# Optimization experiments

Hardware: AMD Instinct MI355X
Metric: run time of the kernel (lower is better)

## Reference

```python
import jax, jax.numpy as jnp
import numpy as np

NV = 100000   # vehicle nodes
NE = 100000   # 'edge' nodes (dst type)
E = 250000    # graph edges (connects relation)
VDIM = 16
EDIM = 16
HID = 128
HEADS = 4
DH = 128      # out_feats per head (GATv2Conv(hid, hid))
EPS = 1e-5
NEG_SLOPE = 0.2


def _layernorm(x, g, b):
    mu = x.mean(-1, keepdims=True)
    var = ((x - mu) ** 2).mean(-1, keepdims=True)
    return (x - mu) * jax.lax.rsqrt(var + EPS) * g + b


def setup_inputs() -> dict:
    key = jax.random.key(0)
    ks = jax.random.split(key, 20)
    s = 0.05
    return {
        "v_feat": jax.random.normal(ks[0], (NV, VDIM), jnp.float32),
        "e_feat": jax.random.normal(ks[1], (NE, EDIM), jnp.float32),
        "Wv": jax.random.normal(ks[2], (VDIM, HID), jnp.float32) * s,
        "bv": jnp.zeros((HID,), jnp.float32),
        "gv": jnp.ones((HID,), jnp.float32),
        "betav": jnp.zeros((HID,), jnp.float32),
        "We": jax.random.normal(ks[3], (EDIM, HID), jnp.float32) * s,
        "be": jnp.zeros((HID,), jnp.float32),
        "ge": jnp.ones((HID,), jnp.float32),
        "betae": jnp.zeros((HID,), jnp.float32),
        "Wsrc": jax.random.normal(ks[4], (HID, HEADS * DH), jnp.float32) * s,
        "bsrc": jnp.zeros((HEADS * DH,), jnp.float32),
        "Wdst": jax.random.normal(ks[5], (HID, HEADS * DH), jnp.float32) * s,
        "bdst": jnp.zeros((HEADS * DH,), jnp.float32),
        "attn": jax.random.normal(ks[6], (HEADS, DH), jnp.float32) * s,
        "Wp": jax.random.normal(ks[7], (HID, HID), jnp.float32) * s,
        "bp": jnp.zeros((HID,), jnp.float32),
        "src": jax.random.randint(ks[8], (E,), 0, NV, jnp.int32),
        "dst": jax.random.randint(ks[9], (E,), 0, NE, jnp.int32),
    }


def reference(v_feat, e_feat, Wv, bv, gv, betav, We, be, ge, betae,
              Wsrc, bsrc, Wdst, bdst, attn, Wp, bp, src, dst):
    # --- node-type encoders: Linear -> ReLU -> LayerNorm ---
    h_v = _layernorm(jax.nn.relu(v_feat @ Wv + bv), gv, betav)      # [NV, HID]
    h_e = _layernorm(jax.nn.relu(e_feat @ We + be), ge, betae)      # [NE, HID]

    # --- GATv2Conv (bipartite: vehicle -> edge), 4 heads ---
    fs = (h_v @ Wsrc + bsrc).reshape(NV, HEADS, DH)                 # src proj
    fd = (h_e @ Wdst + bdst).reshape(NE, HEADS, DH)                 # dst proj
    e = jax.nn.leaky_relu(fs[src] + fd[dst], NEG_SLOPE)             # [E, H, D]
    score = jnp.einsum("ehd,hd->eh", e, attn)                       # [E, H]
    # segment-wise (per-dst-node) softmax over incoming edges
    smax = jax.ops.segment_max(score, dst, num_segments=NE)         # [NE, H]
    ex = jnp.exp(score - smax[dst])
    denom = jax.ops.segment_sum(ex, dst, num_segments=NE)
    alpha = ex / denom[dst]                                         # [E, H]
    out = jax.ops.segment_sum(alpha[:, :, None] * fs[src], dst,
                              num_segments=NE)                      # [NE, H, D]

    # HeteroGraphConv mean-aggregate (single relation -> identity),
    # then mean over heads (edge_out.dim()==3 branch)
    edge_out = out.mean(axis=1)                                     # [NE, HID]

    # feature_proj: Linear -> ReLU -> Dropout(eval: identity)
    return jax.nn.relu(edge_out @ Wp + bp)
```

## Files before the change

kernel.cpp:

```cpp
#include <hip/hip_runtime.h>
#include <hip/hip_bf16.h>
#include <math.h>

#define NV 100000
#define NE_N 100000
#define NEDGE 250000
#define NPAD 100032
#define NEG 0.2f
#define LN_EPS 1e-5f

typedef __bf16 bf16_t;
typedef __bf16 bf16x8 __attribute__((ext_vector_type(8)));
typedef float f32x4 __attribute__((ext_vector_type(4)));
typedef float f32x2 __attribute__((ext_vector_type(2)));

__device__ inline unsigned short f2bfu(float f) {
    return __builtin_bit_cast(unsigned short, (__bf16)f);
}
__device__ inline float blo(unsigned w) { return __uint_as_float(w << 16); }
__device__ inline float bhi(unsigned w) { return __uint_as_float(w & 0xffff0000u); }
__device__ inline float lrelu(float x) { return x > 0.f ? x : NEG * x; }
__device__ inline unsigned pk2(float a, float b) {
    return (unsigned)f2bfu(a) | ((unsigned)f2bfu(b) << 16);
}

__device__ __forceinline__ void gload_lds16(const void* g, void* l) {
    __builtin_amdgcn_global_load_lds(
        (const __attribute__((address_space(1))) unsigned int*)g,
        (__attribute__((address_space(3))) unsigned int*)l,
        16, 0, 0);
}

__global__ __launch_bounds__(256) void prep_kernel(
    const float* __restrict__ Wsrc, const float* __restrict__ Wdst,
    const float* __restrict__ Wp, bf16_t* __restrict__ pS,
    bf16_t* __restrict__ pD, bf16_t* __restrict__ pP,
    int* __restrict__ deg)
{
    int t = blockIdx.x * 256 + threadIdx.x;
    if (t < 8192) {
        int ksq = t >> 9, col = t & 511;
#pragma unroll
        for (int j = 0; j < 8; ++j)
            pS[(size_t)t * 8 + j] = (bf16_t)Wsrc[(ksq * 8 + j) * 512 + col];
    } else if (t < 16384) {
        int g = t - 8192;
        int ksq = g >> 9, col = g & 511;
#pragma unroll
        for (int j = 0; j < 8; ++j)
            pD[(size_t)g * 8 + j] = (bf16_t)Wdst[(ksq * 8 + j) * 512 + col];
    } else if (t < 18432) {
        int g = t - 16384;
        int ksq = g >> 7, col = g & 127;
#pragma unroll
        for (int j = 0; j < 8; ++j)
            pP[(size_t)g * 8 + j] = (bf16_t)Wp[(ksq * 8 + j) * 128 + col];
    } else {
        int z = t - 18432;
        if (z < NE_N) deg[z] = 0;
    }
}

__global__ __launch_bounds__(256) void count_kernel(
    const int* __restrict__ dst, int* __restrict__ deg)
{
    int t = blockIdx.x * 256 + threadIdx.x;
    if (t < NEDGE) atomicAdd(&deg[dst[t]], 1);
}

__global__ __launch_bounds__(256) void scan1_kernel(
    const int* __restrict__ deg, int* __restrict__ offs, int* __restrict__ bsum)
{
    __shared__ int s[256];
    int i = blockIdx.x * 256 + threadIdx.x;
    int v = (i < NE_N) ? deg[i] : 0;
    s[threadIdx.x] = v;
    __syncthreads();
    for (int off = 1; off < 256; off <<= 1) {
        int t_ = (threadIdx.x >= off) ? s[threadIdx.x - off] : 0;
        __syncthreads();
        s[threadIdx.x] += t_;
        __syncthreads();
    }
    if (i < NE_N) offs[i] = s[threadIdx.x] - v;
    if (threadIdx.x == 255) bsum[blockIdx.x] = s[255];
}

__global__ __launch_bounds__(512) void scan2_kernel(int* __restrict__ bsum, int nb)
{
    __shared__ int s[512];
    int t = threadIdx.x;
    int v = (t < nb) ? bsum[t] : 0;
    s[t] = v;
    __syncthreads();
    for (int off = 1; off < 512; off <<= 1) {
        int t_ = (t >= off) ? s[t - off] : 0;
        __syncthreads();
        s[t] += t_;
        __syncthreads();
    }
    if (t < nb) bsum[t] = s[t] - v;
}

__global__ __launch_bounds__(256) void scan3_kernel(
    int* __restrict__ offs, const int* __restrict__ bsum,
    int* __restrict__ cursor, const int* __restrict__ deg,
    int2* __restrict__ od)
{
    int i = blockIdx.x * 256 + threadIdx.x;
    if (i < NE_N) {
        int o = offs[i] + bsum[blockIdx.x];
        offs[i] = o;
        cursor[i] = o;
        od[i] = make_int2(o, deg[i]);
    }
}

__global__ __launch_bounds__(256) void scatter_kernel(
    const int* __restrict__ dst, const int* __restrict__ src,
    int* __restrict__ cursor, int* __restrict__ srcs)
{
    int t = blockIdx.x * 256 + threadIdx.x;
    if (t < NEDGE) {
        int pos = atomicAdd(&cursor[dst[t]], 1);
        srcs[pos] = src[t];
    }
}

__global__ __launch_bounds__(256, 4) void enc_proj_kernel(
    const float* __restrict__ featV, const float* __restrict__ WencV,
    const float* __restrict__ bencV, const float* __restrict__ gV,
    const float* __restrict__ betaV, const bf16_t* __restrict__ ApackV,
    const float* __restrict__ bprojV, unsigned short* __restrict__ outV,
    const float* __restrict__ featE, const float* __restrict__ WencE,
    const float* __restrict__ bencE, const float* __restrict__ gE,
    const float* __restrict__ betaE, const bf16_t* __restrict__ ApackE,
    const float* __restrict__ bprojE, unsigned short* __restrict__ outE,
    int nblk1, int M)
{
    __shared__ unsigned short Hs[64 * 136];
    __shared__ __align__(16) unsigned short Abuf[2][8192];
    __shared__ __align__(16) float Bias[512];

    int b = blockIdx.x;
    bool isV = b < nblk1;
    const float* feat  = isV ? featV  : featE;
    const float* Wenc  = isV ? WencV  : WencE;
    const float* benc  = isV ? bencV  : bencE;
    const float* gln   = isV ? gV     : gE;
    const float* beta  = isV ? betaV  : betaE;
    const bf16_t* Apack = isV ? ApackV : ApackE;
    const float* bproj = isV ? bprojV : bprojE;
    unsigned short* out = isV ? outV : outE;
    int row0 = (isV ? b : b - nblk1) * 64;

    int t = threadIdx.x;
    int l = t & 63;
    int w = t >> 6;
    int rbase = __builtin_amdgcn_readfirstlane(w * 16);

    {
        int sr = row0 + rbase + (l >> 2);
        if (sr > M - 1) sr = M - 1;
        gload_lds16(feat + (size_t)sr * 16 + (l & 3) * 4, &Abuf[1][w * 512]);
    }

#pragma unroll
    for (int j = 0; j < 4; ++j) {
        int ksq = w * 4 + j;
        gload_lds16(Apack + ((size_t)(ksq * 512) + l) * 8, &Abuf[0][ksq * 512]);
    }
    if (t < 128)
        *(float4*)&Bias[t * 4] = *(const float4*)(bproj + t * 4);

    f32x2 wc2[16];
#pragma unroll
    for (int k = 0; k < 16; ++k) {
        float2 wv = *(const float2*)(Wenc + k * 128 + 2 * l);
        wc2[k][0] = wv.x;
        wc2[k][1] = wv.y;
    }
    float2 bv2 = *(const float2*)(benc + 2 * l);

    asm volatile("s_waitcnt vmcnt(0)" ::: "memory");

    const float* Fs = (const float*)&Abuf[1][0];
#pragma unroll
    for (int i = 0; i < 16; ++i) {
        const float* fr = Fs + (rbase + i) * 16;
        float4 f0 = *(const float4*)(fr);
        float4 f1 = *(const float4*)(fr + 4);
        float4 f2 = *(const float4*)(fr + 8);
        float4 f3 = *(const float4*)(fr + 12);
        f32x2 a = {bv2.x, bv2.y};
        a = __builtin_elementwise_fma((f32x2)f0.x, wc2[0],  a);
        a = __builtin_elementwise_fma((f32x2)f0.y, wc2[1],  a);
        a = __builtin_elementwise_fma((f32x2)f0.z, wc2[2],  a);
        a = __builtin_elementwise_fma((f32x2)f0.w, wc2[3],  a);
        a = __builtin_elementwise_fma((f32x2)f1.x, wc2[4],  a);
        a = __builtin_elementwise_fma((f32x2)f1.y, wc2[5],  a);
        a = __builtin_elementwise_fma((f32x2)f1.z, wc2[6],  a);
        a = __builtin_elementwise_fma((f32x2)f1.w, wc2[7],  a);
        a = __builtin_elementwise_fma((f32x2)f2.x, wc2[8],  a);
        a = __builtin_elementwise_fma((f32x2)f2.y, wc2[9],  a);
        a = __builtin_elementwise_fma((f32x2)f2.z, wc2[10], a);
        a = __builtin_elementwise_fma((f32x2)f2.w, wc2[11], a);
        a = __builtin_elementwise_fma((f32x2)f3.x, wc2[12], a);
        a = __builtin_elementwise_fma((f32x2)f3.y, wc2[13], a);
        a = __builtin_elementwise_fma((f32x2)f3.z, wc2[14], a);
        a = __builtin_elementwise_fma((f32x2)f3.w, wc2[15], a);
        float a0 = fmaxf(a[0], 0.f);
        float a1 = fmaxf(a[1], 0.f);
        *(unsigned*)&Hs[(rbase + i) * 136 + 2 * l] = pk2(a0, a1);
    }

    float s = 0.f, s2 = 0.f;
    {
        int rr = rbase + (l >> 2);
        int q = l & 3;
#pragma unroll
        for (int j = 0; j < 4; ++j) {
            uint4 v = *(const uint4*)&Hs[rr * 136 + q * 32 + j * 8];
            float x;
            x = blo(v.x); s += x; s2 = fmaf(x, x, s2);
            x = bhi(v.x); s += x; s2 = fmaf(x, x, s2);
            x = blo(v.y); s += x; s2 = fmaf(x, x, s2);
            x = bhi(v.y); s += x; s2 = fmaf(x, x, s2);
            x = blo(v.z); s += x; s2 = fmaf(x, x, s2);
            x = bhi(v.z); s += x; s2 = fmaf(x, x, s2);
            x = blo(v.w); s += x; s2 = fmaf(x, x, s2);
            x = bhi(v.w); s += x; s2 = fmaf(x, x, s2);
        }
    }
    s  += __shfl_xor(s, 1, 64);  s  += __shfl_xor(s, 2, 64);
    s2 += __shfl_xor(s2, 1, 64); s2 += __shfl_xor(s2, 2, 64);
    float mu  = s * (1.f / 128.f);
    float var = s2 * (1.f / 128.f) - mu * mu;
    float inv = rsqrtf(var + LN_EPS);

    int kq = l >> 4;
    int ln = l & 15;
    float mu_r  = __shfl(mu,  ln * 4, 64);
    float inv_r = __shfl(inv, ln * 4, 64);

    bf16x8 bfr[4];
#pragma unroll
    for (int ks = 0; ks < 4; ++ks) {
        int c0 = ks * 32 + kq * 8;
        uint4 v = *(const uint4*)&Hs[(rbase + ln) * 136 + c0];
        float4 g0 = *(const float4*)(gln + c0);
        float4 g1 = *(const float4*)(gln + c0 + 4);
        float4 b0 = *(const float4*)(beta + c0);
        float4 b1 = *(const float4*)(beta + c0 + 4);
        uint4 p;
        p.x = pk2(fmaf((blo(v.x) - mu_r) * inv_r, g0.x, b0.x),
                  fmaf((bhi(v.x) - mu_r) * inv_r, g0.y, b0.y));
        p.y = pk2(fmaf((blo(v.y) - mu_r) * inv_r, g0.z, b0.z),
                  fmaf((bhi(v.y) - mu_r) * inv_r, g0.w, b0.w));
        p.z = pk2(fmaf((blo(v.z) - mu_r) * inv_r, g1.x, b1.x),
                  fmaf((bhi(v.z) - mu_r) * inv_r, g1.y, b1.y));
        p.w = pk2(fmaf((blo(v.w) - mu_r) * inv_r, g1.z, b1.z),
                  fmaf((bhi(v.w) - mu_r) * inv_r, g1.w, b1.w));
        bfr[ks] = __builtin_bit_cast(bf16x8, p);
    }

    unsigned short* stag = Hs + rbase * 136;
    int node = row0 + rbase + ln;

#pragma unroll
    for (int p = 0; p < 8; ++p) {
        if (p == 0)
            asm volatile("s_waitcnt lgkmcnt(0)" ::: "memory");
        else
            asm volatile("s_waitcnt vmcnt(2)" ::: "memory");
        __builtin_amdgcn_s_barrier();

        if (p < 7) {
#pragma unroll
            for (int j = 0; j < 4; ++j) {
                int ksq = w * 4 + j;
                gload_lds16(Apack + ((size_t)(ksq * 512 + (p + 1) * 64) + l) * 8,
                            &Abuf[(p + 1) & 1][ksq * 512]);
            }
            __builtin_amdgcn_sched_barrier(0);
        }

        const unsigned short* Ac = Abuf[p & 1];
#pragma unroll
        for (int mt = 0; mt < 4; ++mt) {
            bf16x8 a[4];
#pragma unroll
            for (int ks = 0; ks < 4; ++ks)
                a[ks] = *(const bf16x8*)&Ac[((ks * 4 + kq) * 64 + mt * 16 + ln) * 8];

            f32x4 acc = {0.f, 0.f, 0.f, 0.f};
#pragma unroll
            for (int ks = 0; ks < 4; ++ks)
                acc = __builtin_amdgcn_mfma_f32_16x16x32_bf16(a[ks], bfr[ks], acc, 0, 0, 0);

            int colp = p * 64 + mt * 16 + kq * 4;
            float4 bb = *(const float4*)&Bias[colp];
            ushort4 o;
            o.x = f2bfu(acc[0] + bb.x);
            o.y = f2bfu(acc[1] + bb.y);
            o.z = f2bfu(acc[2] + bb.z);
            o.w = f2bfu(acc[3] + bb.w);
            *(ushort4*)&stag[ln * 136 + mt * 16 + kq * 4] = o;
        }
#pragma unroll
        for (int i = 0; i < 2; ++i) {
            uint4 v = *(const uint4*)&stag[ln * 136 + i * 32 + kq * 8];
            *(uint4*)(out + (size_t)node * 512 + p * 64 + i * 32 + kq * 8) = v;
        }
    }
}

__global__ __launch_bounds__(256) void final_gemm_kernel(
    const float* __restrict__ A, const unsigned short* __restrict__ Abf,
    const bf16_t* __restrict__ Ppack, const float* __restrict__ bp,
    float* __restrict__ C, int M)
{
    __shared__ unsigned short Hs[64 * 136];
    int t = threadIdx.x;
    int lane = t & 63;
    int w = t >> 6;
    int row0 = blockIdx.x * 64;

    if (Abf) {
#pragma unroll
        for (int i = 0; i < 4; ++i) {
            int idx = i * 256 + t;
            int r = idx >> 4;
            int c = (idx & 15) * 8;
            uint4 v = make_uint4(0, 0, 0, 0);
            if (row0 + r < M)
                v = *(const uint4*)(Abf + (size_t)(row0 + r) * 128 + c);
            *(uint4*)&Hs[r * 136 + c] = v;
        }
    } else {
#pragma unroll
        for (int i = 0; i < 8; ++i) {
            int f4 = i * 256 + t;
            int r = f4 >> 5;
            int c4 = (f4 & 31) * 4;
            float4 v = make_float4(0.f, 0.f, 0.f, 0.f);
            if (row0 + r < M)
                v = ((const float4*)(A + (size_t)(row0 + r) * 128))[f4 & 31];
            ushort4 o;
            o.x = f2bfu(v.x); o.y = f2bfu(v.y); o.z = f2bfu(v.z); o.w = f2bfu(v.w);
            *(ushort4*)&Hs[r * 136 + c4] = o;
        }
    }
    __syncthreads();

    int kq = lane >> 4;
    int ln = lane & 15;

    f32x4 acc[2][4];
#pragma unroll
    for (int mt = 0; mt < 2; ++mt)
#pragma unroll
        for (int nt = 0; nt < 4; ++nt) {
            f32x4 z = {0.f, 0.f, 0.f, 0.f};
            acc[mt][nt] = z;
        }

#pragma unroll
    for (int ks = 0; ks < 4; ++ks) {
        bf16x8 bfr[4];
#pragma unroll
        for (int nt = 0; nt < 4; ++nt) {
            const uint4* p = (const uint4*)&Hs[(nt * 16 + ln) * 136 + ks * 32 + kq * 8];
            bfr[nt] = __builtin_bit_cast(bf16x8, *p);
        }
        bf16x8 afr[2];
#pragma unroll
        for (int mt = 0; mt < 2; ++mt) {
            int colA = w * 32 + mt * 16 + ln;
            afr[mt] = *(const bf16x8*)(Ppack + ((size_t)(ks * 4 + kq) * 128 + colA) * 8);
        }
#pragma unroll
        for (int mt = 0; mt < 2; ++mt)
#pragma unroll
            for (int nt = 0; nt < 4; ++nt)
                acc[mt][nt] = __builtin_amdgcn_mfma_f32_16x16x32_bf16(
                    afr[mt], bfr[nt], acc[mt][nt], 0, 0, 0);
    }

#pragma unroll
    for (int mt = 0; mt < 2; ++mt) {
        int col = w * 32 + mt * 16 + kq * 4;
        float4 bb = *(const float4*)(bp + col);
#pragma unroll
        for (int nt = 0; nt < 4; ++nt) {
            int node = row0 + nt * 16 + ln;
            if (node < M) {
                float4 o;
                o.x = fmaxf(acc[mt][nt][0] + bb.x, 0.f);
                o.y = fmaxf(acc[mt][nt][1] + bb.y, 0.f);
                o.z = fmaxf(acc[mt][nt][2] + bb.z, 0.f);
                o.w = fmaxf(acc[mt][nt][3] + bb.w, 0.f);
                *(float4*)(C + (size_t)node * 128 + col) = o;
            }
        }
    }
}

__global__ __launch_bounds__(256) void softagg_kernel(
    const unsigned short* __restrict__ fs, const unsigned short* __restrict__ fdp,
    const float* __restrict__ attn, const int2* __restrict__ od,
    const int* __restrict__ srcs, float* __restrict__ outf,
    unsigned short* __restrict__ eo)
{
    int d = blockIdx.x * 4 + (threadIdx.x >> 6);
    if (d >= NE_N) return;
    int l = threadIdx.x & 63;
    int2 rd = od[d];
    int r0 = rd.x;
    int n  = rd.y;
    int o = l * 8;

    uint4 fv = *(const uint4*)(fdp + (size_t)d * 512 + o);
    float fdv[8] = { blo(fv.x), bhi(fv.x), blo(fv.y), bhi(fv.y),
                     blo(fv.z), bhi(fv.z), blo(fv.w), bhi(fv.w) };
    float4 w0 = *(const float4*)(attn + o);
    float4 w1 = *(const float4*)(attn + o + 4);
    float wv[8] = { w0.x, w0.y, w0.z, w0.w, w1.x, w1.y, w1.z, w1.w };

    float m = -1e30f, sm = 0.f;
    float acc[8];
#pragma unroll
    for (int j = 0; j < 8; ++j) acc[j] = 0.f;

    for (int base = 0; base < n; base += 64) {
        int cnt = min(n - base, 64);
        int sl = 0;
        if (l < cnt) sl = srcs[r0 + base + l];
        for (int i = 0; i < cnt; ++i) {
            int s = __shfl(sl, i, 64);
            uint4 a = *(const uint4*)(fs + (size_t)s * 512 + o);
            float fsv[8] = { blo(a.x), bhi(a.x), blo(a.y), bhi(a.y),
                             blo(a.z), bhi(a.z), blo(a.w), bhi(a.w) };
            float p = 0.f;
#pragma unroll
            for (int j = 0; j < 8; ++j)
                p = fmaf(lrelu(fsv[j] + fdv[j]), wv[j], p);
#pragma unroll
            for (int mk = 1; mk < 16; mk <<= 1)
                p += __shfl_xor(p, mk, 64);
            float mn = fmaxf(m, p);
            float c  = __expf(m - mn);
            float av = __expf(p - mn);
            sm = sm * c + av;
            m = mn;
#pragma unroll
            for (int j = 0; j < 8; ++j)
                acc[j] = fmaf(av, fsv[j], acc[j] * c);
        }
    }

    float inv = (n > 0) ? 0.25f / sm : 0.f;
#pragma unroll
    for (int j = 0; j < 8; ++j) {
        float v = acc[j] * inv;
        v += __shfl_xor(v, 16, 64);
        v += __shfl_xor(v, 32, 64);
        acc[j] = v;
    }
    if (l < 16) {
        if (eo) {
            uint4 pk;
            pk.x = pk2(acc[0], acc[1]);
            pk.y = pk2(acc[2], acc[3]);
            pk.z = pk2(acc[4], acc[5]);
            pk.w = pk2(acc[6], acc[7]);
            *(uint4*)(eo + (size_t)d * 128 + l * 8) = pk;
        } else {
            float4 o0 = make_float4(acc[0], acc[1], acc[2], acc[3]);
            float4 o1 = make_float4(acc[4], acc[5], acc[6], acc[7]);
            *(float4*)(outf + (size_t)d * 128 + l * 8) = o0;
            *(float4*)(outf + (size_t)d * 128 + l * 8 + 4) = o1;
        }
    }
}

extern "C" void kernel_launch(void* const* d_in, const int* in_sizes, int n_in,
                              void* d_out, int out_size, void* d_ws, size_t ws_size,
                              hipStream_t stream)
{
    const float* v_feat = (const float*)d_in[0];
    const float* e_feat = (const float*)d_in[1];
    const float* Wv     = (const float*)d_in[2];
    const float* bv     = (const float*)d_in[3];
    const float* gv     = (const float*)d_in[4];
    const float* betav  = (const float*)d_in[5];
    const float* We     = (const float*)d_in[6];
    const float* be     = (const float*)d_in[7];
    const float* ge     = (const float*)d_in[8];
    const float* betae  = (const float*)d_in[9];
    const float* Wsrc   = (const float*)d_in[10];
    const float* bsrc   = (const float*)d_in[11];
    const float* Wdst   = (const float*)d_in[12];
    const float* bdst   = (const float*)d_in[13];
    const float* attn   = (const float*)d_in[14];
    const float* Wp     = (const float*)d_in[15];
    const float* bp     = (const float*)d_in[16];
    const int*   src    = (const int*)d_in[17];
    const int*   dst    = (const int*)d_in[18];
    float* out = (float*)d_out;

    unsigned short* fs = (unsigned short*)d_ws;
    unsigned short* fd = fs + (size_t)NPAD * 512;
    int* deg    = (int*)(fd + (size_t)NPAD * 512);
    int* offs   = deg + NE_N;
    int* cursor = offs + NE_N;
    int* bsum   = cursor + NE_N;
    int2* od    = (int2*)(bsum + 512);
    int* srcs   = (int*)(od + NE_N);
    bf16_t* pS  = (bf16_t*)(srcs + NEDGE);
    bf16_t* pD  = pS + 65536;
    bf16_t* pP  = pD + 65536;
    unsigned short* eo = (unsigned short*)(pP + 16384);

    size_t need = (size_t)((char*)(eo + (size_t)NE_N * 128) - (char*)d_ws);
    if (ws_size < need) eo = nullptr;

    const int NB_SCAN = (NE_N + 255) / 256;

    prep_kernel<<<463, 256, 0, stream>>>(Wsrc, Wdst, Wp, pS, pD, pP, deg);

    count_kernel<<<(NEDGE + 255) / 256, 256, 0, stream>>>(dst, deg);
    scan1_kernel<<<NB_SCAN, 256, 0, stream>>>(deg, offs, bsum);
    scan2_kernel<<<1, 512, 0, stream>>>(bsum, NB_SCAN);
    scan3_kernel<<<NB_SCAN, 256, 0, stream>>>(offs, bsum, cursor, deg, od);
    scatter_kernel<<<(NEDGE + 255) / 256, 256, 0, stream>>>(dst, src, cursor, srcs);

    enc_proj_kernel<<<3126, 256, 0, stream>>>(
        v_feat, Wv, bv, gv, betav, pS, bsrc, fs,
        e_feat, We, be, ge, betae, pD, bdst, fd,
        1563, 100000);

    softagg_kernel<<<NE_N / 4, 256, 0, stream>>>(fs, fd, attn, od, srcs,
                                                 out, eo);

    final_gemm_kernel<<<1563, 256, 0, stream>>>(out, eo, pP, bp, out, NE_N);
}
```

Measured before the change: 287.0 us.

## Restructure encoder projection GEMM to stream weights from registers per wave

The projection stage of the fused encoder kernel is reorganised. Previously each wave kept its 16 rows of activations as the B operand and all waves shared weight tiles staged through double-buffered LDS. Now every wave holds all 64 activation rows in registers and loads its own 128-column slice of the weight directly from global memory, software-prefetching the next tile into registers. This removes the large LDS weight buffers and the per-step barriers, and LayerNorm is applied in place in LDS using register-held values. The cost is more registers (occupancy hint lowered from 4 to 3), redundant weight reads from global/L2 across blocks, and added __syncthreads.

```diff
diff --git a/kernel.cpp b/kernel.cpp
--- a/kernel.cpp
+++ b/kernel.cpp
@@ -127,7 +127,7 @@
     }
 }
 
-__global__ __launch_bounds__(256, 4) void enc_proj_kernel(
+__global__ __launch_bounds__(256, 3) void enc_proj_kernel(
     const float* __restrict__ featV, const float* __restrict__ WencV,
     const float* __restrict__ bencV, const float* __restrict__ gV,
     const float* __restrict__ betaV, const bf16_t* __restrict__ ApackV,
@@ -139,7 +139,7 @@
     int nblk1, int M)
 {
     __shared__ unsigned short Hs[64 * 136];
-    __shared__ __align__(16) unsigned short Abuf[2][8192];
+    __shared__ __align__(16) unsigned short Fbuf[2048];
     __shared__ __align__(16) float Bias[512];
 
     int b = blockIdx.x;
@@ -162,13 +162,7 @@
     {
         int sr = row0 + rbase + (l >> 2);
         if (sr > M - 1) sr = M - 1;
-        gload_lds16(feat + (size_t)sr * 16 + (l & 3) * 4, &Abuf[1][w * 512]);
-    }
-
-#pragma unroll
-    for (int j = 0; j < 4; ++j) {
-        int ksq = w * 4 + j;
-        gload_lds16(Apack + ((size_t)(ksq * 512) + l) * 8, &Abuf[0][ksq * 512]);
+        gload_lds16(feat + (size_t)sr * 16 + (l & 3) * 4, &Fbuf[w * 512]);
     }
     if (t < 128)
         *(float4*)&Bias[t * 4] = *(const float4*)(bproj + t * 4);
@@ -181,10 +175,13 @@
         wc2[k][1] = wv.y;
     }
     float2 bv2 = *(const float2*)(benc + 2 * l);
+    float2 g2  = *(const float2*)(gln + 2 * l);
+    float2 be2 = *(const float2*)(beta + 2 * l);
 
     asm volatile("s_waitcnt vmcnt(0)" ::: "memory");
 
-    const float* Fs = (const float*)&Abuf[1][0];
+    const float* Fs = (const float*)&Fbuf[0];
+    float ar0[16], ar1[16];
 #pragma unroll
     for (int i = 0; i < 16; ++i) {
         const float* fr = Fs + (rbase + i) * 16;
@@ -211,6 +208,8 @@
         a = __builtin_elementwise_fma((f32x2)f3.w, wc2[15], a);
         float a0 = fmaxf(a[0], 0.f);
         float a1 = fmaxf(a[1], 0.f);
+        ar0[i] = a0;
+        ar1[i] = a1;
         *(unsigned*)&Hs[(rbase + i) * 136 + 2 * l] = pk2(a0, a1);
     }
 
@@ -238,79 +237,85 @@
     float var = s2 * (1.f / 128.f) - mu * mu;
     float inv = rsqrtf(var + LN_EPS);
 
+#pragma unroll
+    for (int i = 0; i < 16; ++i) {
+        float mu_i  = __shfl(mu,  4 * i, 64);
+        float inv_i = __shfl(inv, 4 * i, 64);
+        float n0 = fmaf((ar0[i] - mu_i) * inv_i, g2.x, be2.x);
+        float n1 = fmaf((ar1[i] - mu_i) * inv_i, g2.y, be2.y);
+        *(unsigned*)&Hs[(rbase + i) * 136 + 2 * l] = pk2(n0, n1);
+    }
+
+    __syncthreads();
+
     int kq = l >> 4;
     int ln = l & 15;
-    float mu_r  = __shfl(mu,  ln * 4, 64);
-    float inv_r = __shfl(inv, ln * 4, 64);
-
-    bf16x8 bfr[4];
-#pragma unroll
-    for (int ks = 0; ks < 4; ++ks) {
-        int c0 = ks * 32 + kq * 8;
-        uint4 v = *(const uint4*)&Hs[(rbase + ln) * 136 + c0];
-        float4 g0 = *(const float4*)(gln + c0);
-        float4 g1 = *(const float4*)(gln + c0 + 4);
-        float4 b0 = *(const float4*)(beta + c0);
-        float4 b1 = *(const float4*)(beta + c0 + 4);
-        uint4 p;
-        p.x = pk2(fmaf((blo(v.x) - mu_r) * inv_r, g0.x, b0.x),
-                  fmaf((bhi(v.x) - mu_r) * inv_r, g0.y, b0.y));
-        p.y = pk2(fmaf((blo(v.y) - mu_r) * inv_r, g0.z, b0.z),
-                  fmaf((bhi(v.y) - mu_r) * inv_r, g0.w, b0.w));
-        p.z = pk2(fmaf((blo(v.z) - mu_r) * inv_r, g1.x, b1.x),
-                  fmaf((bhi(v.z) - mu_r) * inv_r, g1.y, b1.y));
-        p.w = pk2(fmaf((blo(v.w) - mu_r) * inv_r, g1.z, b1.z),
-                  fmaf((bhi(v.w) - mu_r) * inv_r, g1.w, b1.w));
-        bfr[ks] = __builtin_bit_cast(bf16x8, p);
-    }
-
-    unsigned short* stag = Hs + rbase * 136;
-    int node = row0 + rbase + ln;
-
-#pragma unroll
-    for (int p = 0; p < 8; ++p) {
-        if (p == 0)
-            asm volatile("s_waitcnt lgkmcnt(0)" ::: "memory");
-        else
-            asm volatile("s_waitcnt vmcnt(2)" ::: "memory");
-        __builtin_amdgcn_s_barrier();
-
-        if (p < 7) {
-#pragma unroll
-            for (int j = 0; j < 4; ++j) {
-                int ksq = w * 4 + j;
-                gload_lds16(Apack + ((size_t)(ksq * 512 + (p + 1) * 64) + l) * 8,
-                            &Abuf[(p + 1) & 1][ksq * 512]);
+    bf16x8 bfr[4][4];
+#pragma unroll
+    for (int rt = 0; rt < 4; ++rt)
+#pragma unroll
+        for (int ks = 0; ks < 4; ++ks)
+            bfr[rt][ks] = __builtin_bit_cast(bf16x8,
+                *(const uint4*)&Hs[(rt * 16 + ln) * 136 + ks * 32 + kq * 8]);
+
+    __syncthreads();
+
+    unsigned short* stw = Hs + w * 2176;
+    int cb = w * 128 + ln;
+
+    bf16x8 ac[4], an[4];
+#pragma unroll
+    for (int ks = 0; ks < 4; ++ks)
+        ac[ks] = *(const bf16x8*)(Apack + ((size_t)((ks * 4 + kq) * 512) + cb) * 8);
+
+#pragma unroll
+    for (int mt = 0; mt < 8; ++mt) {
+        if (mt < 7) {
+#pragma unroll
+            for (int ks = 0; ks < 4; ++ks)
+                an[ks] = *(const bf16x8*)(Apack +
+                    ((size_t)((ks * 4 + kq) * 512) + cb + (mt + 1) * 16) * 8);
+        }
+
+        f32x4 acc[4];
+#pragma unroll
+        for (int rt = 0; rt < 4; ++rt) {
+            f32x4 z = {0.f, 0.f, 0.f, 0.f};
+            acc[rt] = z;
+        }
+#pragma unroll
+        for (int ks = 0; ks < 4; ++ks)
+#pragma unroll
+            for (int rt = 0; rt < 4; ++rt)
+                acc[rt] = __builtin_amdgcn_mfma_f32_16x16x32_bf16(
+                    ac[ks], bfr[rt][ks], acc[rt], 0, 0, 0);
+
+        int colp = w * 128 + mt * 16 + kq * 4;
+        float4 bb = *(const float4*)&Bias[colp];
+#pragma unroll
+        for (int rt = 0; rt < 4; ++rt) {
+            ushort4 o;
+            o.x = f2bfu(acc[rt][0] + bb.x);
+            o.y = f2bfu(acc[rt][1] + bb.y);
+            o.z = f2bfu(acc[rt][2] + bb.z);
+            o.w = f2bfu(acc[rt][3] + bb.w);
+            *(ushort4*)&stw[(rt * 16 + ln) * 34 + (mt & 1) * 16 + kq * 4] = o;
+        }
+
+        if (mt & 1) {
+            int bc = w * 128 + (mt - 1) * 16;
+#pragma unroll
+            for (int i = 0; i < 4; ++i) {
+                int r = i * 16 + (l >> 2);
+                uint4 v = *(const uint4*)&stw[r * 34 + (l & 3) * 8];
+                *(uint4*)(out + (size_t)(row0 + r) * 512 + bc + (l & 3) * 8) = v;
             }
-            __builtin_amdgcn_sched_barrier(0);
-        }
-
-        const unsigned short* Ac = Abuf[p & 1];
-#pragma unroll
-        for (int mt = 0; mt < 4; ++mt) {
-            bf16x8 a[4];
+        }
+
+        if (mt < 7) {
 #pragma unroll
             for (int ks = 0; ks < 4; ++ks)
-                a[ks] = *(const bf16x8*)&Ac[((ks * 4 + kq) * 64 + mt * 16 + ln) * 8];
-
-            f32x4 acc = {0.f, 0.f, 0.f, 0.f};
-#pragma unroll
-            for (int ks = 0; ks < 4; ++ks)
-                acc = __builtin_amdgcn_mfma_f32_16x16x32_bf16(a[ks], bfr[ks], acc, 0, 0, 0);
-
-            int colp = p * 64 + mt * 16 + kq * 4;
-            float4 bb = *(const float4*)&Bias[colp];
-            ushort4 o;
-            o.x = f2bfu(acc[0] + bb.x);
-            o.y = f2bfu(acc[1] + bb.y);
-            o.z = f2bfu(acc[2] + bb.z);
-            o.w = f2bfu(acc[3] + bb.w);
-            *(ushort4*)&stag[ln * 136 + mt * 16 + kq * 4] = o;
-        }
-#pragma unroll
-        for (int i = 0; i < 2; ++i) {
-            uint4 v = *(const uint4*)&stag[ln * 136 + i * 32 + kq * 8];
-            *(uint4*)(out + (size_t)node * 512 + p * 64 + i * 32 + kq * 8) = v;
+                ac[ks] = an[ks];
         }
     }
 }
```

New measurement: 318.0 us. +10.8%, slower.

## Replace three-pass scan with atomic block reservation; batch gathers via LDS loads

Applied to the files above, without the earlier changes.

The three-kernel exclusive scan over destination degrees becomes one kernel. Each block scans locally and reserves a contiguous range with a single atomicAdd on a global counter, so two launches and the offs/bsum round trips go away. Segment order across blocks becomes nondeterministic, but each segment stays contiguous, which is all the CSR needs. In softagg, source-row gathers are now issued in groups of four as direct global-to-LDS loads, followed by one wait, to keep more memory requests in flight. That adds an LDS round trip and a full vmcnt(0) stall per group.

```diff
diff --git a/kernel.cpp b/kernel.cpp
--- a/kernel.cpp
+++ b/kernel.cpp
@@ -35,9 +35,10 @@
     const float* __restrict__ Wsrc, const float* __restrict__ Wdst,
     const float* __restrict__ Wp, bf16_t* __restrict__ pS,
     bf16_t* __restrict__ pD, bf16_t* __restrict__ pP,
-    int* __restrict__ deg)
+    int* __restrict__ deg, int* __restrict__ gctr)
 {
     int t = blockIdx.x * 256 + threadIdx.x;
+    if (t == 0) *gctr = 0;
     if (t < 8192) {
         int ksq = t >> 9, col = t & 511;
 #pragma unroll
@@ -68,10 +69,12 @@
     if (t < NEDGE) atomicAdd(&deg[dst[t]], 1);
 }
 
-__global__ __launch_bounds__(256) void scan1_kernel(
-    const int* __restrict__ deg, int* __restrict__ offs, int* __restrict__ bsum)
+__global__ __launch_bounds__(256) void reserve_kernel(
+    const int* __restrict__ deg, int* __restrict__ cursor,
+    int2* __restrict__ od, int* __restrict__ gctr)
 {
     __shared__ int s[256];
+    __shared__ int base;
     int i = blockIdx.x * 256 + threadIdx.x;
     int v = (i < NE_N) ? deg[i] : 0;
     s[threadIdx.x] = v;
@@ -82,37 +85,12 @@
         s[threadIdx.x] += t_;
         __syncthreads();
     }
-    if (i < NE_N) offs[i] = s[threadIdx.x] - v;
-    if (threadIdx.x == 255) bsum[blockIdx.x] = s[255];
-}
-
-__global__ __launch_bounds__(512) void scan2_kernel(int* __restrict__ bsum, int nb)
-{
-    __shared__ int s[512];
-    int t = threadIdx.x;
-    int v = (t < nb) ? bsum[t] : 0;
-    s[t] = v;
+    if (threadIdx.x == 255) base = atomicAdd(gctr, s[255]);
     __syncthreads();
-    for (int off = 1; off < 512; off <<= 1) {
-        int t_ = (t >= off) ? s[t - off] : 0;
-        __syncthreads();
-        s[t] += t_;
-        __syncthreads();
-    }
-    if (t < nb) bsum[t] = s[t] - v;
-}
-
-__global__ __launch_bounds__(256) void scan3_kernel(
-    int* __restrict__ offs, const int* __restrict__ bsum,
-    int* __restrict__ cursor, const int* __restrict__ deg,
-    int2* __restrict__ od)
-{
-    int i = blockIdx.x * 256 + threadIdx.x;
     if (i < NE_N) {
-        int o = offs[i] + bsum[blockIdx.x];
-        offs[i] = o;
+        int o = base + s[threadIdx.x] - v;
         cursor[i] = o;
-        od[i] = make_int2(o, deg[i]);
+        od[i] = make_int2(o, v);
     }
 }
 
@@ -412,7 +390,9 @@
     const int* __restrict__ srcs, float* __restrict__ outf,
     unsigned short* __restrict__ eo)
 {
-    int d = blockIdx.x * 4 + (threadIdx.x >> 6);
+    __shared__ __align__(16) unsigned short Ebuf[4][4][512];
+    int wq = threadIdx.x >> 6;
+    int d = blockIdx.x * 4 + wq;
     if (d >= NE_N) return;
     int l = threadIdx.x & 63;
     int2 rd = od[d];
@@ -436,26 +416,33 @@
         int cnt = min(n - base, 64);
         int sl = 0;
         if (l < cnt) sl = srcs[r0 + base + l];
-        for (int i = 0; i < cnt; ++i) {
-            int s = __shfl(sl, i, 64);
-            uint4 a = *(const uint4*)(fs + (size_t)s * 512 + o);
-            float fsv[8] = { blo(a.x), bhi(a.x), blo(a.y), bhi(a.y),
-                             blo(a.z), bhi(a.z), blo(a.w), bhi(a.w) };
-            float p = 0.f;
-#pragma unroll
-            for (int j = 0; j < 8; ++j)
-                p = fmaf(lrelu(fsv[j] + fdv[j]), wv[j], p);
-#pragma unroll
-            for (int mk = 1; mk < 16; mk <<= 1)
-                p += __shfl_xor(p, mk, 64);
-            float mn = fmaxf(m, p);
-            float c  = __expf(m - mn);
-            float av = __expf(p - mn);
-            sm = sm * c + av;
-            m = mn;
-#pragma unroll
-            for (int j = 0; j < 8; ++j)
-                acc[j] = fmaf(av, fsv[j], acc[j] * c);
+        for (int c0 = 0; c0 < cnt; c0 += 4) {
+            int mc = min(4, cnt - c0);
+            for (int j = 0; j < mc; ++j) {
+                int s = __shfl(sl, c0 + j, 64);
+                gload_lds16(fs + (size_t)s * 512 + l * 8, &Ebuf[wq][j][0]);
+            }
+            asm volatile("s_waitcnt vmcnt(0)" ::: "memory");
+            for (int j = 0; j < mc; ++j) {
+                uint4 a = *(const uint4*)&Ebuf[wq][j][o];
+                float fsv[8] = { blo(a.x), bhi(a.x), blo(a.y), bhi(a.y),
+                                 blo(a.z), bhi(a.z), blo(a.w), bhi(a.w) };
+                float p = 0.f;
+#pragma unroll
+                for (int jj = 0; jj < 8; ++jj)
+                    p = fmaf(lrelu(fsv[jj] + fdv[jj]), wv[jj], p);
+#pragma unroll
+                for (int mk = 1; mk < 16; mk <<= 1)
+                    p += __shfl_xor(p, mk, 64);
+                float mn = fmaxf(m, p);
+                float c  = __expf(m - mn);
+                float av = __expf(p - mn);
+                sm = sm * c + av;
+                m = mn;
+#pragma unroll
+                for (int jj = 0; jj < 8; ++jj)
+                    acc[jj] = fmaf(av, fsv[jj], acc[jj] * c);
+            }
         }
     }
 
@@ -512,10 +499,9 @@
     unsigned short* fs = (unsigned short*)d_ws;
     unsigned short* fd = fs + (size_t)NPAD * 512;
     int* deg    = (int*)(fd + (size_t)NPAD * 512);
-    int* offs   = deg + NE_N;
-    int* cursor = offs + NE_N;
-    int* bsum   = cursor + NE_N;
-    int2* od    = (int2*)(bsum + 512);
+    int* cursor = deg + NE_N;
+    int* gctr   = cursor + NE_N;
+    int2* od    = (int2*)(gctr + 4);
     int* srcs   = (int*)(od + NE_N);
     bf16_t* pS  = (bf16_t*)(srcs + NEDGE);
     bf16_t* pD  = pS + 65536;
@@ -527,12 +513,10 @@
 
     const int NB_SCAN = (NE_N + 255) / 256;
 
-    prep_kernel<<<463, 256, 0, stream>>>(Wsrc, Wdst, Wp, pS, pD, pP, deg);
+    prep_kernel<<<463, 256, 0, stream>>>(Wsrc, Wdst, Wp, pS, pD, pP, deg, gctr);
 
     count_kernel<<<(NEDGE + 255) / 256, 256, 0, stream>>>(dst, deg);
-    scan1_kernel<<<NB_SCAN, 256, 0, stream>>>(deg, offs, bsum);
-    scan2_kernel<<<1, 512, 0, stream>>>(bsum, NB_SCAN);
-    scan3_kernel<<<NB_SCAN, 256, 0, stream>>>(offs, bsum, cursor, deg, od);
+    reserve_kernel<<<NB_SCAN, 256, 0, stream>>>(deg, cursor, od, gctr);
     scatter_kernel<<<(NEDGE + 255) / 256, 256, 0, stream>>>(dst, src, cursor, srcs);
 
     enc_proj_kernel<<<3126, 256, 0, stream>>>(
```

After: 296.4 us. +3.3%, slower.
